# Kernel tuning notes

Hardware: AMD Instinct MI355X
Metric: run time of the kernel (lower is better)

The kernel has to match this reference:

```python
import jax, jax.numpy as jnp
import numpy as np

N = 50000      # nodes
E = 1600000    # edges
D = 128        # input_dim
H = 128        # hidden_dim
C = 10         # n_class
G = 512        # number of graphs (max(idx)+1)
LRELU_ALPHA = 0.05
BN_EPS = 1e-5


def setup_inputs() -> dict:
    key = jax.random.key(0)
    ks = jax.random.split(key, 10)
    x_in = jax.random.normal(ks[0], (N, D), dtype=jnp.float32)
    edge_index = jax.random.randint(ks[1], (2, E), 0, N, dtype=jnp.int32)
    idx = jnp.sort(jax.random.randint(ks[2], (N,), 0, G, dtype=jnp.int32))

    def lin(k, shape, fan_in):
        return jax.random.normal(k, shape, dtype=jnp.float32) / np.sqrt(fan_in).astype(np.float32)

    fc_w = lin(ks[3], (H, D), D)        # GATLayer.fc weight
    a1 = lin(ks[4], (H,), 2 * H)        # a weight, src half
    a2 = lin(ks[5], (H,), 2 * H)        # a weight, dst half
    fc1_w = lin(ks[6], (H, H), H)
    fc1_b = jnp.zeros((H,), jnp.float32)
    fc2_w = lin(ks[7], (C, H), H)
    fc2_b = jnp.zeros((C,), jnp.float32)
    gamma = jnp.ones((H,), jnp.float32)  # BatchNorm weight
    beta = jnp.zeros((H,), jnp.float32)  # BatchNorm bias
    return {"x_in": x_in, "edge_index": edge_index, "idx": idx,
            "fc_w": fc_w, "a1": a1, "a2": a2,
            "fc1_w": fc1_w, "fc1_b": fc1_b, "fc2_w": fc2_w, "fc2_b": fc2_b,
            "gamma": gamma, "beta": beta}


def reference(x_in, edge_index, idx, fc_w, a1, a2, fc1_w, fc1_b, fc2_w, fc2_b, gamma, beta):
    # input standardization (torch.std is unbiased -> ddof=1)
    x = (x_in - jnp.mean(x_in)) / jnp.std(x_in, ddof=1)

    # ---- GAT layer ----
    z = x @ fc_w.T                              # [N, H]
    src, dst = edge_index[0], edge_index[1]
    # a([z_src ; z_dst]) == z_src@a1 + z_dst@a2  (avoids materializing [E, 2H])
    s1 = z @ a1                                  # [N]
    s2 = z @ a2                                  # [N]
    e = s1[src] + s2[dst]                        # [E]
    e = jnp.where(e >= 0, e, LRELU_ALPHA * e)    # LeakyReLU(0.05)
    h = jnp.exp(e)
    h_sum = jax.ops.segment_sum(h, src, num_segments=N)   # edge-softmax denom per src row
    alpha = h / h_sum[src]                       # [E]
    # sparse.mm(adj_att, z): out[src] += alpha * z[dst]
    out = jax.ops.segment_sum(alpha[:, None] * z[dst], src, num_segments=N)  # [N, H]

    x = jax.nn.relu(out)
    # dropout: identity (eval / deterministic reference)

    # sum pooling per graph
    pooled = jax.ops.segment_sum(x, idx, num_segments=G)   # [G, H]

    # BatchNorm1d (training-mode batch statistics, biased var)
    mu = jnp.mean(pooled, axis=0)
    var = jnp.var(pooled, axis=0)
    xb = (pooled - mu) / jnp.sqrt(var + BN_EPS) * gamma + beta

    x = jax.nn.relu(xb @ fc1_w.T + fc1_b)
    logits = x @ fc2_w.T + fc2_b
    return jax.nn.log_softmax(logits, axis=1)
```

## Files before the change

### kernel.cpp

```cpp
#include <hip/hip_runtime.h>

#define NN 50000
#define NE 1600000
#define DD 128
#define HH 128
#define CC 10
#define GG 512
#define LRELU_A 0.05f
#define BN_EPS 1e-5f

#define TT 256
#define EPT (NE / TT)
#define NBR 782
#define NBP 784
#define NPB 64
#define KNODE 8
#define STB 1024

typedef unsigned int u32;
typedef unsigned short u16;
typedef unsigned char u8;

__device__ __forceinline__ u16 f2bf(float f) {
    u32 u = __float_as_uint(f);
    u32 r = u + 0x7FFFu + ((u >> 16) & 1u);
    return (u16)(r >> 16);
}

__global__ __launch_bounds__(256) void k_front(const int* __restrict__ src,
                                               const float* __restrict__ x,
                                               u16* __restrict__ cnt_b,
                                               u8* __restrict__ rank_e,
                                               float* __restrict__ pooled,
                                               double* __restrict__ pst) {
    __shared__ u32 h[NBP];
    __shared__ double ls[4], lss[4];
    int bid = blockIdx.x, tid = threadIdx.x;
    if (bid < TT) {
        for (int i = tid; i < NBP; i += 256) h[i] = 0;
        pooled[bid * 256 + tid] = 0.f;
        __syncthreads();
        int e0 = bid * EPT;
        for (int i = tid; i < EPT; i += 256) {
            int b = src[e0 + i] >> 6;
            u32 old = atomicAdd(&h[b], 1u);
            rank_e[e0 + i] = (u8)old;
        }
        __syncthreads();
        for (int i = tid; i < NBP; i += 256) cnt_b[bid * NBP + i] = (u16)h[i];
    } else {
        int sb = bid - TT;
        const int M4 = NN * DD / 4;
        double s = 0.0, ss = 0.0;
        for (int i = sb * 256 + tid; i < M4; i += STB * 256) {
            float4 v = reinterpret_cast<const float4*>(x)[i];
            s  += (double)v.x + (double)v.y + (double)v.z + (double)v.w;
            ss += (double)v.x * v.x + (double)v.y * v.y + (double)v.z * v.z +
                  (double)v.w * v.w;
        }
        for (int d = 32; d; d >>= 1) { s += __shfl_down(s, d); ss += __shfl_down(ss, d); }
        int lane = tid & 63, w = tid >> 6;
        if (lane == 0) { ls[w] = s; lss[w] = ss; }
        __syncthreads();
        if (tid == 0) {
            pst[2 * sb]     = ls[0] + ls[1] + ls[2] + ls[3];
            pst[2 * sb + 1] = lss[0] + lss[1] + lss[2] + lss[3];
        }
    }
}

__global__ __launch_bounds__(256) void k_mid(const u16* __restrict__ cnt_b,
                                             const double* __restrict__ pst,
                                             const float* __restrict__ fc_w,
                                             u16* __restrict__ rel_b,
                                             int* __restrict__ base_b,
                                             float* __restrict__ wsum,
                                             float* __restrict__ musig,
                                             float* __restrict__ wt) {
    int t = threadIdx.x;
    int bid = blockIdx.x;
    if (bid == 0) {
        __shared__ int sm[256];
        __shared__ int runs;
        if (t == 0) runs = 0;
        __syncthreads();
        for (int chunk = 0; chunk < 4; ++chunk) {
            int b = chunk * 256 + t;
            int tot = 0;
            if (b < NBP)
                for (int tt = 0; tt < TT; ++tt) tot += cnt_b[tt * NBP + b];
            sm[t] = tot;
            __syncthreads();
            for (int d = 1; d < 256; d <<= 1) {
                int x = 0;
                if (t >= d) x = sm[t - d];
                __syncthreads();
                if (t >= d) sm[t] += x;
                __syncthreads();
            }
            if (b < NBP) base_b[b] = runs + sm[t] - tot;
            __syncthreads();
            if (t == 255) runs += sm[255];
            __syncthreads();
        }
        if (t == 0) base_b[NBP] = runs;
    } else if (bid <= 4) {
        int b = (bid - 1) * 196 + t;
        if (t < 196) {
            int run = 0;
            for (int tt = 0; tt < TT; ++tt) {
                int c = cnt_b[tt * NBP + b];
                rel_b[tt * NBP + b] = (u16)run;
                run += c;
            }
        }
    } else {
        __shared__ double rs[256], rss[256];
        double s  = pst[2 * t] + pst[2 * (t + 256)] + pst[2 * (t + 512)] + pst[2 * (t + 768)];
        double ss = pst[2 * t + 1] + pst[2 * (t + 256) + 1] +
                    pst[2 * (t + 512) + 1] + pst[2 * (t + 768) + 1];
        rs[t] = s; rss[t] = ss;
        __syncthreads();
        for (int d = 128; d; d >>= 1) {
            if (t < d) { rs[t] += rs[t + d]; rss[t] += rss[t + d]; }
            __syncthreads();
        }
        if (t == 0) {
            double M = (double)NN * DD;
            double mean = rs[0] / M;
            double var  = (rss[0] - rs[0] * rs[0] / M) / (M - 1.0);
            musig[0] = (float)mean;
            musig[1] = (float)(1.0 / sqrt(var));
        }
        if (t < 128) {
            float acc = 0.f;
            for (int k = 0; k < DD; ++k) acc += fc_w[t * DD + k];
            wsum[t] = acc;
        }
        for (int i = t; i < DD * HH; i += 256) {
            int k = i >> 7, c = i & 127;
            wt[i] = fc_w[c * DD + k];
        }
    }
}

#define PADX 132
__global__ __launch_bounds__(256, 2) void k_big(const int* __restrict__ src,
                                                const int* __restrict__ dst,
                                                const u16* __restrict__ rel_b,
                                                const u8* __restrict__ rank_e,
                                                const int* __restrict__ base_b,
                                                u32* __restrict__ ebuf,
                                                const float* __restrict__ x,
                                                const float* __restrict__ wt,
                                                const float* __restrict__ wsum,
                                                const float* __restrict__ musig,
                                                const float* __restrict__ a1,
                                                const float* __restrict__ a2,
                                                u32* __restrict__ zbf,
                                                float* __restrict__ s1,
                                                float* __restrict__ s2) {
    __shared__ float xs[128][PADX];
    int bid = blockIdx.x, tid = threadIdx.x;

    if (bid < TT) {
        int e0 = bid * EPT;
        for (int i = tid; i < EPT; i += 256) {
            int s = src[e0 + i];
            int b = s >> 6;
            int pos = base_b[b] + (int)rel_b[bid * NBP + b] + (int)rank_e[e0 + i];
            ebuf[pos] = ((u32)dst[e0 + i] << 6) | (u32)(s & 63);
        }
        return;
    }

    int row0 = (bid - TT) * 128;
    for (int i = tid; i < 128 * 32; i += 256) {
        int r = i >> 5;
        int m = i & 31;
        int gr = row0 + r;
        float4 v = (gr < NN) ? reinterpret_cast<const float4*>(x)[gr * 32 + m]
                             : make_float4(0.f, 0.f, 0.f, 0.f);
        *reinterpret_cast<float4*>(&xs[r][m << 2]) = v;
    }
    __syncthreads();

    int trow = tid >> 4, tcol = tid & 15;
    float acc[8][8];
    #pragma unroll
    for (int i = 0; i < 8; ++i)
        #pragma unroll
        for (int j = 0; j < 8; ++j) acc[i][j] = 0.f;

    const float4* wt4 = reinterpret_cast<const float4*>(wt);
    for (int k = 0; k < 128; k += 4) {
        float4 xv[8];
        #pragma unroll
        for (int i = 0; i < 8; ++i)
            xv[i] = *reinterpret_cast<const float4*>(&xs[trow * 8 + i][k]);
        #pragma unroll
        for (int kk = 0; kk < 4; ++kk) {
            float4 w0 = wt4[(k + kk) * 32 + tcol * 2];
            float4 w1 = wt4[(k + kk) * 32 + tcol * 2 + 1];
            #pragma unroll
            for (int i = 0; i < 8; ++i) {
                float a = (kk == 0) ? xv[i].x
                        : (kk == 1) ? xv[i].y
                        : (kk == 2) ? xv[i].z : xv[i].w;
                acc[i][0] += a * w0.x; acc[i][1] += a * w0.y;
                acc[i][2] += a * w0.z; acc[i][3] += a * w0.w;
                acc[i][4] += a * w1.x; acc[i][5] += a * w1.y;
                acc[i][6] += a * w1.z; acc[i][7] += a * w1.w;
            }
        }
    }

    float mu = musig[0], isig = musig[1];
    int c0 = tcol * 8;
    float4 a10 = *reinterpret_cast<const float4*>(&a1[c0]);
    float4 a11 = *reinterpret_cast<const float4*>(&a1[c0 + 4]);
    float4 a20 = *reinterpret_cast<const float4*>(&a2[c0]);
    float4 a21 = *reinterpret_cast<const float4*>(&a2[c0 + 4]);
    float ws0x = wsum[c0 + 0], ws0y = wsum[c0 + 1], ws0z = wsum[c0 + 2], ws0w = wsum[c0 + 3];
    float ws1x = wsum[c0 + 4], ws1y = wsum[c0 + 5], ws1z = wsum[c0 + 6], ws1w = wsum[c0 + 7];

    float p1[8], p2[8];
    #pragma unroll
    for (int i = 0; i < 8; ++i) {
        int gr = row0 + trow * 8 + i;
        float4 o0, o1;
        o0.x = (acc[i][0] - mu * ws0x) * isig;
        o0.y = (acc[i][1] - mu * ws0y) * isig;
        o0.z = (acc[i][2] - mu * ws0z) * isig;
        o0.w = (acc[i][3] - mu * ws0w) * isig;
        o1.x = (acc[i][4] - mu * ws1x) * isig;
        o1.y = (acc[i][5] - mu * ws1y) * isig;
        o1.z = (acc[i][6] - mu * ws1z) * isig;
        o1.w = (acc[i][7] - mu * ws1w) * isig;
        p1[i] = o0.x * a10.x + o0.y * a10.y + o0.z * a10.z + o0.w * a10.w +
                o1.x * a11.x + o1.y * a11.y + o1.z * a11.z + o1.w * a11.w;
        p2[i] = o0.x * a20.x + o0.y * a20.y + o0.z * a20.z + o0.w * a20.w +
                o1.x * a21.x + o1.y * a21.y + o1.z * a21.z + o1.w * a21.w;
        if (gr < NN) {
            uint4 pk;
            pk.x = ((u32)f2bf(o0.y) << 16) | f2bf(o0.x);
            pk.y = ((u32)f2bf(o0.w) << 16) | f2bf(o0.z);
            pk.z = ((u32)f2bf(o1.y) << 16) | f2bf(o1.x);
            pk.w = ((u32)f2bf(o1.w) << 16) | f2bf(o1.z);
            *reinterpret_cast<uint4*>(&zbf[gr * 64 + tcol * 4]) = pk;
        }
    }
    #pragma unroll
    for (int d = 8; d; d >>= 1) {
        #pragma unroll
        for (int i = 0; i < 8; ++i) {
            p1[i] += __shfl_down(p1[i], d, 16);
            p2[i] += __shfl_down(p2[i], d, 16);
        }
    }
    if (tcol == 0) {
        #pragma unroll
        for (int i = 0; i < 8; ++i) {
            int gr = row0 + trow * 8 + i;
            if (gr < NN) { s1[gr] = p1[i]; s2[gr] = p2[i]; }
        }
    }
}

__global__ __launch_bounds__(256) void k_bcsr(const u32* __restrict__ ebuf,
                                              const int* __restrict__ base_b,
                                              const float* __restrict__ s1,
                                              const float* __restrict__ s2,
                                              int* __restrict__ off,
                                              u32* __restrict__ dst_s) {
    __shared__ u32 hist[NPB];
    __shared__ u32 cur[NPB];
    __shared__ int sm[NPB];
    int b = blockIdx.x, tid = threadIdx.x;
    int ebase = base_b[b], eend = base_b[b + 1];
    int m = eend - ebase;
    if (tid < NPB) hist[tid] = 0;
    __syncthreads();
    for (int i = tid; i < m; i += 256)
        atomicAdd(&hist[ebuf[ebase + i] & 63u], 1u);
    __syncthreads();
    if (tid < NPB) sm[tid] = (int)hist[tid];
    __syncthreads();
    for (int d = 1; d < NPB; d <<= 1) {
        int x = 0;
        if (tid < NPB && tid >= d) x = sm[tid - d];
        __syncthreads();
        if (tid < NPB && tid >= d) sm[tid] += x;
        __syncthreads();
    }
    if (tid < NPB) {
        int v = (int)hist[tid];
        int st = sm[tid] - v;
        cur[tid] = (u32)st;
        int n = b * NPB + tid;
        if (n < NN) off[n] = ebase + st;
    }
    if (b == NBR - 1 && tid == 0) off[NN] = NE;
    __syncthreads();
    for (int i = tid; i < m; i += 256) {
        u32 e = ebuf[ebase + i];
        int ls = (int)(e & 63u);
        int dn = (int)(e >> 6);
        int p = (int)atomicAdd(&cur[ls], 1u);
        float ev = s1[b * NPB + ls] + s2[dn];
        ev = (ev >= 0.f) ? ev : LRELU_A * ev;
        float h = __expf(ev);
        dst_s[ebase + p] = ((u32)dn << 16) | (u32)f2bf(h);
    }
}

__global__ __launch_bounds__(256) void k_aggregate(const u32* __restrict__ zbf,
                                                   const int* __restrict__ off,
                                                   const u32* __restrict__ dst_s,
                                                   const int* __restrict__ idx,
                                                   float* __restrict__ pooled) {
    int wave = (blockIdx.x * 256 + threadIdx.x) >> 6;
    int lane = threadIdx.x & 63;
    int n0 = wave * KNODE;
    if (n0 >= NN) return;
    int n1 = n0 + KNODE;
    if (n1 > NN) n1 = NN;

    float pool0 = 0.f, pool1 = 0.f;
    int curg = idx[n0];

    for (int node = n0; node < n1; ++node) {
        int g = idx[node];
        if (g != curg) {
            atomicAdd(&pooled[curg * HH + lane * 2], pool0);
            atomicAdd(&pooled[curg * HH + lane * 2 + 1], pool1);
            pool0 = 0.f; pool1 = 0.f;
            curg = g;
        }
        int j0 = off[node], j1 = off[node + 1];
        float acc0 = 0.f, acc1 = 0.f, hsl = 0.f;

        for (int b = j0; b < j1; b += 64) {
            int cnt = j1 - b;
            if (cnt > 64) cnt = 64;
            int jj = b + ((lane < cnt) ? lane : 0);
            int ul = (int)dst_s[jj];
            if (lane < cnt) hsl += __uint_as_float((u32)ul << 16);
            int k = 0;
            for (; k + 8 <= cnt; k += 8) {
                int eu[8]; u32 uu[8];
                #pragma unroll
                for (int q = 0; q < 8; ++q) eu[q] = __shfl(ul, k + q);
                #pragma unroll
                for (int q = 0; q < 8; ++q)
                    uu[q] = zbf[(((u32)eu[q] >> 16) << 6) | lane];
                #pragma unroll
                for (int q = 0; q < 8; ++q) {
                    float hq = __uint_as_float((u32)eu[q] << 16);
                    acc0 += hq * __uint_as_float(uu[q] << 16);
                    acc1 += hq * __uint_as_float(uu[q] & 0xFFFF0000u);
                }
            }
            for (; k + 4 <= cnt; k += 4) {
                int eu[4]; u32 uu[4];
                #pragma unroll
                for (int q = 0; q < 4; ++q) eu[q] = __shfl(ul, k + q);
                #pragma unroll
                for (int q = 0; q < 4; ++q)
                    uu[q] = zbf[(((u32)eu[q] >> 16) << 6) | lane];
                #pragma unroll
                for (int q = 0; q < 4; ++q) {
                    float hq = __uint_as_float((u32)eu[q] << 16);
                    acc0 += hq * __uint_as_float(uu[q] << 16);
                    acc1 += hq * __uint_as_float(uu[q] & 0xFFFF0000u);
                }
            }
            for (; k < cnt; ++k) {
                int e = __shfl(ul, k);
                float hk = __uint_as_float((u32)e << 16);
                u32 u = zbf[(((u32)e >> 16) << 6) | lane];
                acc0 += hk * __uint_as_float(u << 16);
                acc1 += hk * __uint_as_float(u & 0xFFFF0000u);
            }
        }
        float hs = hsl;
        #pragma unroll
        for (int d = 32; d; d >>= 1) hs += __shfl_xor(hs, d);
        float inv = (hs > 0.f) ? 1.f / hs : 0.f;
        pool0 += fmaxf(acc0 * inv, 0.f);
        pool1 += fmaxf(acc1 * inv, 0.f);
    }
    atomicAdd(&pooled[curg * HH + lane * 2], pool0);
    atomicAdd(&pooled[curg * HH + lane * 2 + 1], pool1);
}

__global__ __launch_bounds__(128) void k_head(const float* __restrict__ pooled,
                                              const float* __restrict__ gamma,
                                              const float* __restrict__ beta,
                                              const float* __restrict__ fc1w,
                                              const float* __restrict__ fc1b,
                                              const float* __restrict__ fc2w,
                                              const float* __restrict__ fc2b,
                                              float* __restrict__ out) {
    __shared__ __align__(16) float xb[128];
    __shared__ __align__(16) float h1[128];
    __shared__ float lg[16];
    int g = blockIdx.x;
    int t = threadIdx.x;
    float s = 0.f, ss = 0.f;
    #pragma unroll 8
    for (int q = 0; q < GG; ++q) {
        float v = pooled[q * HH + t];
        s += v;
        ss += v * v;
    }
    float mean = s / GG;
    float var  = ss / GG - mean * mean;
    float sc = gamma[t] * rsqrtf(var + BN_EPS);
    xb[t] = pooled[g * HH + t] * sc + (beta[t] - mean * sc);
    __syncthreads();
    float acc = 0.f;
    const float4* wr = reinterpret_cast<const float4*>(&fc1w[t * HH]);
    #pragma unroll 8
    for (int k = 0; k < 32; ++k) {
        float4 w4 = wr[k];
        float4 xv = *reinterpret_cast<const float4*>(&xb[k * 4]);
        acc += w4.x * xv.x + w4.y * xv.y + w4.z * xv.z + w4.w * xv.w;
    }
    acc += fc1b[t];
    h1[t] = (acc > 0.f) ? acc : 0.f;
    __syncthreads();
    if (t < CC) {
        float a = 0.f;
        const float4* w2 = reinterpret_cast<const float4*>(&fc2w[t * HH]);
        #pragma unroll 8
        for (int k = 0; k < 32; ++k) {
            float4 w4 = w2[k];
            float4 hv = *reinterpret_cast<const float4*>(&h1[k * 4]);
            a += w4.x * hv.x + w4.y * hv.y + w4.z * hv.z + w4.w * hv.w;
        }
        lg[t] = a + fc2b[t];
    }
    __syncthreads();
    if (t == 0) {
        float mx = lg[0];
        for (int c = 1; c < CC; ++c) mx = fmaxf(mx, lg[c]);
        float se = 0.f;
        for (int c = 0; c < CC; ++c) se += __expf(lg[c] - mx);
        float lse = mx + logf(se);
        for (int c = 0; c < CC; ++c) out[g * CC + c] = lg[c] - lse;
    }
}

extern "C" void kernel_launch(void* const* d_in, const int* in_sizes, int n_in,
                              void* d_out, int out_size, void* d_ws, size_t ws_size,
                              hipStream_t stream) {
    const float* x_in  = (const float*)d_in[0];
    const int*   eidx  = (const int*)d_in[1];
    const int*   src   = eidx;
    const int*   dst   = eidx + NE;
    const int*   idx   = (const int*)d_in[2];
    const float* fc_w  = (const float*)d_in[3];
    const float* a1    = (const float*)d_in[4];
    const float* a2    = (const float*)d_in[5];
    const float* fc1w  = (const float*)d_in[6];
    const float* fc1b  = (const float*)d_in[7];
    const float* fc2w  = (const float*)d_in[8];
    const float* fc2b  = (const float*)d_in[9];
    const float* gamma = (const float*)d_in[10];
    const float* beta  = (const float*)d_in[11];
    float* out = (float*)d_out;

    char* p = (char*)d_ws;
    auto alloc = [&](size_t bytes) {
        char* r = p;
        p += (bytes + 255) & ~(size_t)255;
        return r;
    };
    double* pst    = (double*)alloc((size_t)STB * 2 * sizeof(double));
    float*  wsum   = (float*)alloc(HH * sizeof(float));
    float*  musig  = (float*)alloc(4 * sizeof(float));
    float*  wt     = (float*)alloc((size_t)DD * HH * sizeof(float));
    u16*    cnt_b  = (u16*)alloc((size_t)TT * NBP * sizeof(u16));
    u16*    rel_b  = (u16*)alloc((size_t)TT * NBP * sizeof(u16));
    u8*     rank_e = (u8*)alloc((size_t)NE * sizeof(u8));
    int*    base_b = (int*)alloc((NBP + 1) * sizeof(int));
    u32*    ebuf   = (u32*)alloc((size_t)NE * sizeof(u32));
    int*    off    = (int*)alloc((NN + 1) * sizeof(int));
    u32*    dst_s  = (u32*)alloc((size_t)NE * sizeof(u32));
    u32*    zbf    = (u32*)alloc((size_t)NN * (HH / 2) * sizeof(u32));
    float*  s1     = (float*)alloc(NN * sizeof(float));
    float*  s2     = (float*)alloc(NN * sizeof(float));
    float*  pooled = (float*)alloc((size_t)GG * HH * sizeof(float));

    k_front<<<TT + STB, 256, 0, stream>>>(src, x_in, cnt_b, rank_e, pooled, pst);
    k_mid<<<6, 256, 0, stream>>>(cnt_b, pst, fc_w, rel_b, base_b, wsum, musig, wt);
    int gemm_blocks = (NN + 127) / 128;
    k_big<<<TT + gemm_blocks, 256, 0, stream>>>(src, dst, rel_b, rank_e, base_b,
                                                ebuf, x_in, wt, wsum, musig,
                                                a1, a2, zbf, s1, s2);
    k_bcsr<<<NBR, 256, 0, stream>>>(ebuf, base_b, s1, s2, off, dst_s);
    int nwaves = (NN + KNODE - 1) / KNODE;
    int nblocks = (nwaves + 3) / 4;
    k_aggregate<<<nblocks, 256, 0, stream>>>(zbf, off, dst_s, idx, pooled);
    k_head<<<GG, 128, 0, stream>>>(pooled, gamma, beta, fc1w, fc1b, fc2w, fc2b, out);
}
```

Baseline: 184.1 us.

## Compute node projection GEMM with bf16 MFMA instead of fp32 FMA

Replaces the fp32 register-tiled GEMM in k_big with bf16 MFMA 16x16x32 instructions. The input x is converted to bf16 in LDS, fc_w is stored as bf16 row-major, and the block tile shrinks to 64 rows. The epilogue stages z through LDS so rows are written coalesced and s1/s2 are recomputed from the bf16-rounded z. This cuts the FMA-bound cost of the projection but lowers GEMM input precision to bf16; wsum is made consistent with the rounded weights.

```diff
diff --git a/kernel.cpp b/kernel.cpp
--- a/kernel.cpp
+++ b/kernel.cpp
@@ -20,11 +20,16 @@
 typedef unsigned int u32;
 typedef unsigned short u16;
 typedef unsigned char u8;
+typedef __attribute__((ext_vector_type(8))) short bf16x8;
+typedef __attribute__((ext_vector_type(4))) float f32x4;
 
 __device__ __forceinline__ u16 f2bf(float f) {
     u32 u = __float_as_uint(f);
     u32 r = u + 0x7FFFu + ((u >> 16) & 1u);
     return (u16)(r >> 16);
+}
+__device__ __forceinline__ float bf2f(u32 lo16) {
+    return __uint_as_float(lo16 << 16);
 }
 
 __global__ __launch_bounds__(256) void k_front(const int* __restrict__ src,
@@ -76,7 +81,7 @@
                                              int* __restrict__ base_b,
                                              float* __restrict__ wsum,
                                              float* __restrict__ musig,
-                                             float* __restrict__ wt) {
+                                             u16* __restrict__ wbf) {
     int t = threadIdx.x;
     int bid = blockIdx.x;
     if (bid == 0) {
@@ -132,35 +137,33 @@
             musig[0] = (float)mean;
             musig[1] = (float)(1.0 / sqrt(var));
         }
+        for (int i = t; i < DD * HH; i += 256) wbf[i] = f2bf(fc_w[i]);
         if (t < 128) {
             float acc = 0.f;
-            for (int k = 0; k < DD; ++k) acc += fc_w[t * DD + k];
+            for (int k = 0; k < DD; ++k)
+                acc += bf2f(f2bf(fc_w[t * DD + k]));
             wsum[t] = acc;
         }
-        for (int i = t; i < DD * HH; i += 256) {
-            int k = i >> 7, c = i & 127;
-            wt[i] = fc_w[c * DD + k];
-        }
-    }
-}
-
-#define PADX 132
-__global__ __launch_bounds__(256, 2) void k_big(const int* __restrict__ src,
-                                                const int* __restrict__ dst,
-                                                const u16* __restrict__ rel_b,
-                                                const u8* __restrict__ rank_e,
-                                                const int* __restrict__ base_b,
-                                                u32* __restrict__ ebuf,
-                                                const float* __restrict__ x,
-                                                const float* __restrict__ wt,
-                                                const float* __restrict__ wsum,
-                                                const float* __restrict__ musig,
-                                                const float* __restrict__ a1,
-                                                const float* __restrict__ a2,
-                                                u32* __restrict__ zbf,
-                                                float* __restrict__ s1,
-                                                float* __restrict__ s2) {
-    __shared__ float xs[128][PADX];
+    }
+}
+
+#define XP 136
+__global__ __launch_bounds__(256) void k_big(const int* __restrict__ src,
+                                             const int* __restrict__ dst,
+                                             const u16* __restrict__ rel_b,
+                                             const u8* __restrict__ rank_e,
+                                             const int* __restrict__ base_b,
+                                             u32* __restrict__ ebuf,
+                                             const float* __restrict__ x,
+                                             const u16* __restrict__ wbf,
+                                             const float* __restrict__ wsum,
+                                             const float* __restrict__ musig,
+                                             const float* __restrict__ a1,
+                                             const float* __restrict__ a2,
+                                             u32* __restrict__ zbf,
+                                             float* __restrict__ s1,
+                                             float* __restrict__ s2) {
+    __shared__ u16 xls[64 * XP];
     int bid = blockIdx.x, tid = threadIdx.x;
 
     if (bid < TT) {
@@ -174,96 +177,83 @@
         return;
     }
 
-    int row0 = (bid - TT) * 128;
-    for (int i = tid; i < 128 * 32; i += 256) {
-        int r = i >> 5;
-        int m = i & 31;
+    int row0 = (bid - TT) * 64;
+    for (int i = tid; i < 64 * 32; i += 256) {
+        int r = i >> 5, m = i & 31;
         int gr = row0 + r;
         float4 v = (gr < NN) ? reinterpret_cast<const float4*>(x)[gr * 32 + m]
                              : make_float4(0.f, 0.f, 0.f, 0.f);
-        *reinterpret_cast<float4*>(&xs[r][m << 2]) = v;
-    }
-    __syncthreads();
-
-    int trow = tid >> 4, tcol = tid & 15;
-    float acc[8][8];
+        u32 p0 = ((u32)f2bf(v.y) << 16) | f2bf(v.x);
+        u32 p1 = ((u32)f2bf(v.w) << 16) | f2bf(v.z);
+        *reinterpret_cast<uint2*>(&xls[r * XP + m * 4]) = make_uint2(p0, p1);
+    }
+    __syncthreads();
+
+    int w = tid >> 6, l = tid & 63;
+    int lrow = l & 15, lk = l >> 4;
+
+    bf16x8 af[4];
     #pragma unroll
-    for (int i = 0; i < 8; ++i)
+    for (int kc = 0; kc < 4; ++kc)
+        af[kc] = *reinterpret_cast<const bf16x8*>(
+            &xls[(w * 16 + lrow) * XP + kc * 32 + lk * 8]);
+
+    f32x4 acc[8];
+    #pragma unroll
+    for (int nt = 0; nt < 8; ++nt) acc[nt] = (f32x4){0.f, 0.f, 0.f, 0.f};
+
+    #pragma unroll
+    for (int nt = 0; nt < 8; ++nt) {
         #pragma unroll
-        for (int j = 0; j < 8; ++j) acc[i][j] = 0.f;
-
-    const float4* wt4 = reinterpret_cast<const float4*>(wt);
-    for (int k = 0; k < 128; k += 4) {
-        float4 xv[8];
+        for (int kc = 0; kc < 4; ++kc) {
+            bf16x8 bfr = *reinterpret_cast<const bf16x8*>(
+                &wbf[(nt * 16 + lrow) * DD + kc * 32 + lk * 8]);
+            acc[nt] = __builtin_amdgcn_mfma_f32_16x16x32_bf16(af[kc], bfr,
+                                                              acc[nt], 0, 0, 0);
+        }
+    }
+    __syncthreads();
+
+    float mu = musig[0], isig = musig[1];
+    #pragma unroll
+    for (int nt = 0; nt < 8; ++nt) {
+        int col = nt * 16 + lrow;
+        float wsc = wsum[col];
         #pragma unroll
-        for (int i = 0; i < 8; ++i)
-            xv[i] = *reinterpret_cast<const float4*>(&xs[trow * 8 + i][k]);
+        for (int r = 0; r < 4; ++r) {
+            int lr = w * 16 + lk * 4 + r;
+            float z = (acc[nt][r] - mu * wsc) * isig;
+            xls[lr * XP + col] = f2bf(z);
+        }
+    }
+    __syncthreads();
+
+    {
+        int r = tid >> 2, q = tid & 3;
+        int gr = row0 + r;
+        const uint4* lz = reinterpret_cast<const uint4*>(&xls[r * XP + q * 32]);
+        uint4 c0 = lz[0], c1 = lz[1], c2 = lz[2], c3 = lz[3];
+        if (gr < NN) {
+            uint4* zb = reinterpret_cast<uint4*>(zbf) + gr * 16 + q * 4;
+            zb[0] = c0; zb[1] = c1; zb[2] = c2; zb[3] = c3;
+        }
+        u32 wd[16] = {c0.x, c0.y, c0.z, c0.w, c1.x, c1.y, c1.z, c1.w,
+                      c2.x, c2.y, c2.z, c2.w, c3.x, c3.y, c3.z, c3.w};
+        const float4* A14 = reinterpret_cast<const float4*>(a1 + q * 32);
+        const float4* A24 = reinterpret_cast<const float4*>(a2 + q * 32);
+        float p1 = 0.f, p2 = 0.f;
         #pragma unroll
-        for (int kk = 0; kk < 4; ++kk) {
-            float4 w0 = wt4[(k + kk) * 32 + tcol * 2];
-            float4 w1 = wt4[(k + kk) * 32 + tcol * 2 + 1];
-            #pragma unroll
-            for (int i = 0; i < 8; ++i) {
-                float a = (kk == 0) ? xv[i].x
-                        : (kk == 1) ? xv[i].y
-                        : (kk == 2) ? xv[i].z : xv[i].w;
-                acc[i][0] += a * w0.x; acc[i][1] += a * w0.y;
-                acc[i][2] += a * w0.z; acc[i][3] += a * w0.w;
-                acc[i][4] += a * w1.x; acc[i][5] += a * w1.y;
-                acc[i][6] += a * w1.z; acc[i][7] += a * w1.w;
-            }
-        }
-    }
-
-    float mu = musig[0], isig = musig[1];
-    int c0 = tcol * 8;
-    float4 a10 = *reinterpret_cast<const float4*>(&a1[c0]);
-    float4 a11 = *reinterpret_cast<const float4*>(&a1[c0 + 4]);
-    float4 a20 = *reinterpret_cast<const float4*>(&a2[c0]);
-    float4 a21 = *reinterpret_cast<const float4*>(&a2[c0 + 4]);
-    float ws0x = wsum[c0 + 0], ws0y = wsum[c0 + 1], ws0z = wsum[c0 + 2], ws0w = wsum[c0 + 3];
-    float ws1x = wsum[c0 + 4], ws1y = wsum[c0 + 5], ws1z = wsum[c0 + 6], ws1w = wsum[c0 + 7];
-
-    float p1[8], p2[8];
-    #pragma unroll
-    for (int i = 0; i < 8; ++i) {
-        int gr = row0 + trow * 8 + i;
-        float4 o0, o1;
-        o0.x = (acc[i][0] - mu * ws0x) * isig;
-        o0.y = (acc[i][1] - mu * ws0y) * isig;
-        o0.z = (acc[i][2] - mu * ws0z) * isig;
-        o0.w = (acc[i][3] - mu * ws0w) * isig;
-        o1.x = (acc[i][4] - mu * ws1x) * isig;
-        o1.y = (acc[i][5] - mu * ws1y) * isig;
-        o1.z = (acc[i][6] - mu * ws1z) * isig;
-        o1.w = (acc[i][7] - mu * ws1w) * isig;
-        p1[i] = o0.x * a10.x + o0.y * a10.y + o0.z * a10.z + o0.w * a10.w +
-                o1.x * a11.x + o1.y * a11.y + o1.z * a11.z + o1.w * a11.w;
-        p2[i] = o0.x * a20.x + o0.y * a20.y + o0.z * a20.z + o0.w * a20.w +
-                o1.x * a21.x + o1.y * a21.y + o1.z * a21.z + o1.w * a21.w;
-        if (gr < NN) {
-            uint4 pk;
-            pk.x = ((u32)f2bf(o0.y) << 16) | f2bf(o0.x);
-            pk.y = ((u32)f2bf(o0.w) << 16) | f2bf(o0.z);
-            pk.z = ((u32)f2bf(o1.y) << 16) | f2bf(o1.x);
-            pk.w = ((u32)f2bf(o1.w) << 16) | f2bf(o1.z);
-            *reinterpret_cast<uint4*>(&zbf[gr * 64 + tcol * 4]) = pk;
-        }
-    }
-    #pragma unroll
-    for (int d = 8; d; d >>= 1) {
-        #pragma unroll
-        for (int i = 0; i < 8; ++i) {
-            p1[i] += __shfl_down(p1[i], d, 16);
-            p2[i] += __shfl_down(p2[i], d, 16);
-        }
-    }
-    if (tcol == 0) {
-        #pragma unroll
-        for (int i = 0; i < 8; ++i) {
-            int gr = row0 + trow * 8 + i;
-            if (gr < NN) { s1[gr] = p1[i]; s2[gr] = p2[i]; }
-        }
+        for (int j = 0; j < 8; ++j) {
+            float4 va1 = A14[j], va2 = A24[j];
+            u32 wlo = wd[2 * j], whi = wd[2 * j + 1];
+            float z0 = bf2f(wlo & 0xFFFFu), z1 = bf2f(wlo >> 16);
+            float z2 = bf2f(whi & 0xFFFFu), z3 = bf2f(whi >> 16);
+            p1 += z0 * va1.x + z1 * va1.y + z2 * va1.z + z3 * va1.w;
+            p2 += z0 * va2.x + z1 * va2.y + z2 * va2.z + z3 * va2.w;
+        }
+        p1 += __shfl_down(p1, 2, 4); p1 += __shfl_down(p1, 1, 4);
+        p2 += __shfl_down(p2, 2, 4); p2 += __shfl_down(p2, 1, 4);
+        if (q == 0 && gr < NN) { s1[gr] = p1; s2[gr] = p2; }
     }
 }
 
@@ -480,7 +470,7 @@
     double* pst    = (double*)alloc((size_t)STB * 2 * sizeof(double));
     float*  wsum   = (float*)alloc(HH * sizeof(float));
     float*  musig  = (float*)alloc(4 * sizeof(float));
-    float*  wt     = (float*)alloc((size_t)DD * HH * sizeof(float));
+    u16*    wbf    = (u16*)alloc((size_t)DD * HH * sizeof(u16));
     u16*    cnt_b  = (u16*)alloc((size_t)TT * NBP * sizeof(u16));
     u16*    rel_b  = (u16*)alloc((size_t)TT * NBP * sizeof(u16));
     u8*     rank_e = (u8*)alloc((size_t)NE * sizeof(u8));
@@ -494,10 +484,10 @@
     float*  pooled = (float*)alloc((size_t)GG * HH * sizeof(float));
 
     k_front<<<TT + STB, 256, 0, stream>>>(src, x_in, cnt_b, rank_e, pooled, pst);
-    k_mid<<<6, 256, 0, stream>>>(cnt_b, pst, fc_w, rel_b, base_b, wsum, musig, wt);
-    int gemm_blocks = (NN + 127) / 128;
+    k_mid<<<6, 256, 0, stream>>>(cnt_b, pst, fc_w, rel_b, base_b, wsum, musig, wbf);
+    int gemm_blocks = (NN + 63) / 64;
     k_big<<<TT + gemm_blocks, 256, 0, stream>>>(src, dst, rel_b, rank_e, base_b,
-                                                ebuf, x_in, wt, wsum, musig,
+                                                ebuf, x_in, wbf, wsum, musig,
                                                 a1, a2, zbf, s1, s2);
     k_bcsr<<<NBR, 256, 0, stream>>>(ebuf, base_b, s1, s2, off, dst_s);
     int nwaves = (NN + KNODE - 1) / KNODE;
```

After: 180.9 us. About the same (-1.7%).
